# Kernel tuning notes

Hardware: AMD Instinct MI355X
Metric: run time of the kernel (lower is better)

The kernel has to match this reference:

```python
import jax, jax.numpy as jnp
import numpy as np

VOCAB, EMB, VGG, HID, LAYERS, B, T = 10000, 512, 4096, 512, 2, 128, 25


def setup_inputs() -> dict:
    key = jax.random.key(0)
    ks = jax.random.split(key, 20)
    n0 = HID + EMB   # layer-0 concat size
    n1 = HID + HID   # layer-1 concat size
    inp = {
        "vgg_fc7_features": jax.random.normal(ks[0], (B, VGG), jnp.float32),
        "xTokens": jax.random.randint(ks[1], (B, T), 0, VOCAB),
        "is_train": 1,
        "emb": jax.random.normal(ks[2], (VOCAB, EMB), jnp.float32) * 0.1,
        "W_in": jax.random.normal(ks[3], (VGG, HID), jnp.float32) / np.sqrt(VGG).astype(np.float32),
        "b_in": jnp.zeros((HID,), jnp.float32),
        "Wu0": jax.random.normal(ks[4], (n0, HID), jnp.float32) / np.sqrt(n0).astype(np.float32),
        "bu0": jnp.zeros((HID,), jnp.float32),
        "Wr0": jax.random.normal(ks[5], (n0, HID), jnp.float32) / np.sqrt(n0).astype(np.float32),
        "br0": jnp.zeros((HID,), jnp.float32),
        "Wc0": jax.random.normal(ks[6], (n0, HID), jnp.float32) / np.sqrt(n0).astype(np.float32),
        "bc0": jnp.zeros((HID,), jnp.float32),
        "Wu1": jax.random.normal(ks[7], (n1, HID), jnp.float32) / np.sqrt(n1).astype(np.float32),
        "bu1": jnp.zeros((HID,), jnp.float32),
        "Wr1": jax.random.normal(ks[8], (n1, HID), jnp.float32) / np.sqrt(n1).astype(np.float32),
        "br1": jnp.zeros((HID,), jnp.float32),
        "Wc1": jax.random.normal(ks[9], (n1, HID), jnp.float32) / np.sqrt(n1).astype(np.float32),
        "bc1": jnp.zeros((HID,), jnp.float32),
        "W_out": jax.random.normal(ks[10], (HID, VOCAB), jnp.float32) / np.sqrt(HID).astype(np.float32),
        "b_out": jnp.zeros((VOCAB,), jnp.float32),
    }
    return inp


def _gru(x, h, Wu, bu, Wr, br, Wc, bc):
    xh = jnp.concatenate([x, h], axis=1)
    gu = jax.nn.sigmoid(xh @ Wu + bu)
    gr = jax.nn.sigmoid(xh @ Wr + br)
    hh = jnp.tanh(jnp.concatenate([x, gr * h], axis=1) @ Wc + bc)
    return gu * h + (1.0 - gu) * hh


def reference(vgg_fc7_features, xTokens, is_train, emb, W_in, b_in,
              Wu0, bu0, Wr0, br0, Wc0, bc0,
              Wu1, bu1, Wr1, br1, Wc1, bc1,
              W_out, b_out):
    # initial hidden state from image features, replicated per rnn layer
    h0 = jnp.tanh(vgg_fc7_features @ W_in + b_in)  # [B, HID]
    init = (h0, h0)
    emb_seq = emb[xTokens]               # [B, T, EMB]
    emb_seq = jnp.swapaxes(emb_seq, 0, 1)  # [T, B, EMB]

    def step(carry, x_t):
        s0, s1 = carry
        s0n = _gru(x_t, s0, Wu0, bu0, Wr0, br0, Wc0, bc0)
        s1n = _gru(s0n, s1, Wu1, bu1, Wr1, br1, Wc1, bc1)
        logit = s1n @ W_out + b_out      # [B, VOCAB]
        return (s0n, s1n), logit

    (s0f, s1f), logits = jax.lax.scan(step, init, emb_seq)
    logits = jnp.swapaxes(logits, 0, 1)  # [B, T, VOCAB]
    current_state = jnp.stack([s0f, s1f])  # [LAYERS, B, HID]
    return logits, current_state
```

## Files before the change

### kernel.cpp

```cpp
#include <hip/hip_runtime.h>
#include <hip/hip_bf16.h>

#define BB 128
#define TT 25
#define VOCAB 10000
#define HIDD 512

typedef __hip_bfloat16 bf16;
typedef short bf16x8 __attribute__((ext_vector_type(8)));
typedef float f32x4 __attribute__((ext_vector_type(4)));

__device__ __forceinline__ float sigmoidf_(float x) { return 1.0f / (1.0f + __expf(-x)); }

__device__ __forceinline__ float4 f4_fma(float s, float4 w, float4 a) {
    a.x += s * w.x; a.y += s * w.y; a.z += s * w.z; a.w += s * w.w;
    return a;
}

__device__ __forceinline__ unsigned short f2bfu(float x) {
    bf16 h = __float2bfloat16(x);
    return *reinterpret_cast<unsigned short*>(&h);
}

__device__ __forceinline__ float4 core128(const float* __restrict__ Wp,
                                          const float* __restrict__ arow)
{
    float4 acc = {0.f, 0.f, 0.f, 0.f};
    #pragma unroll 2
    for (int k = 0; k < 128; k += 8) {
        float4 w[8];
        #pragma unroll
        for (int j = 0; j < 8; ++j)
            w[j] = *(const float4*)(Wp + (size_t)(k + j) * 512);
        #pragma unroll
        for (int j = 0; j < 8; ++j)
            acc = f4_fma(arow[k + j], w[j], acc);
    }
    return acc;
}

#define PHASE_REDUCE(SVAR) \
    __syncthreads(); \
    float4 SVAR; \
    if (tid < 32) { \
        SVAR = red[tid]; \
        _Pragma("unroll") \
        for (int j = 1; j < 8; ++j) { \
            float4 p = red[tid + 32 * j]; \
            SVAR.x += p.x; SVAR.y += p.y; SVAR.z += p.z; SVAR.w += p.w; \
        } \
    }

__global__ __launch_bounds__(256) void k_h0p(const float* __restrict__ A,
                                             const float* __restrict__ W,
                                             float* __restrict__ partial)
{
    __shared__ float As2[2][1032];
    __shared__ float4 red[256];
    const int tid = threadIdx.x;
    const int n4 = tid & 15, mi = (tid >> 4) & 1, kh = tid >> 5;
    const int m0 = blockIdx.y * 2, col0 = blockIdx.x * 64, kq = blockIdx.z;

    #pragma unroll
    for (int l = 0; l < 2; ++l) {
        int idx = tid + l * 256;
        int r = idx >> 8, c4 = (idx & 255) * 4;
        *(float4*)&As2[r][c4] =
            *(const float4*)&A[(size_t)(m0 + r) * 4096 + kq * 1024 + c4];
    }
    __syncthreads();
    red[tid] = core128(W + (size_t)(kq * 1024 + kh * 128) * 512 + col0 + n4 * 4,
                       &As2[mi][kh * 128]);
    PHASE_REDUCE(s)
    if (tid < 32) {
        int m = m0 + (tid >> 4), cc = col0 + (tid & 15) * 4;
        *(float4*)&partial[((size_t)kq * 128 + m) * 512 + cc] = s;
    }
}

__global__ void k_h0f(const float* __restrict__ partial,
                      const float* __restrict__ bias,
                      float* __restrict__ s0, float* __restrict__ s1)
{
    int i = blockIdx.x * 256 + threadIdx.x;
    size_t e = (size_t)i * 4;
    int cc = (int)(e & 511);
    float4 s = *(const float4*)&partial[e];
    #pragma unroll
    for (int j = 1; j < 4; ++j) {
        float4 p = *(const float4*)&partial[(size_t)j * 128 * 512 + e];
        s.x += p.x; s.y += p.y; s.z += p.z; s.w += p.w;
    }
    float4 b4 = *(const float4*)&bias[cc];
    float4 o;
    o.x = tanhf(s.x + b4.x); o.y = tanhf(s.y + b4.y);
    o.z = tanhf(s.z + b4.z); o.w = tanhf(s.w + b4.w);
    *(float4*)&s0[e] = o;
    *(float4*)&s1[e] = o;
}

__global__ __launch_bounds__(512, 4) void k_gates(
    const float* __restrict__ h0p, const float* __restrict__ h1p,
    const int* __restrict__ toks, const float* __restrict__ emb, int t,
    const float* __restrict__ Wu0, const float* __restrict__ bu0,
    const float* __restrict__ Wr0, const float* __restrict__ br0,
    const float* __restrict__ Wu1, const float* __restrict__ bu1,
    const float* __restrict__ Wr1, const float* __restrict__ br1,
    float* __restrict__ gu0, float* __restrict__ grh0,
    float* __restrict__ gu1, float* __restrict__ grh1,
    int doL0, int doL1)
{
    __shared__ float As[8 * 1028];
    __shared__ float4 red[8][8][16];
    const int bx = blockIdx.x;
    const int cb = bx & 7, gate = (bx >> 3) & 3, mb = bx >> 5;
    if (gate < 2) { if (!doL0) return; } else { if (!doL1) return; }
    const int col0 = cb * 64, m0 = mb * 8;
    const int tid = threadIdx.x;

    #pragma unroll
    for (int l = 0; l < 4; ++l) {
        int idx = tid + l * 512;
        int r2 = idx >> 7;
        int c4 = (idx & 127) * 4;
        int r = r2 & 7, half = r2 >> 3;
        float4 v;
        if (gate < 2) {
            if (half == 0) {
                int tok = toks[(m0 + r) * TT + t];
                v = *(const float4*)&emb[(size_t)tok * 512 + c4];
            } else {
                v = *(const float4*)&h0p[(size_t)(m0 + r) * 512 + c4];
            }
        } else {
            const float* src = (half == 0) ? h0p : h1p;
            v = *(const float4*)&src[(size_t)(m0 + r) * 512 + c4];
        }
        *(float4*)&As[r * 1028 + half * 512 + c4] = v;
    }
    __syncthreads();

    {
        const int kq = tid >> 6, lane = tid & 63;
        const int n4 = lane & 15, rl = lane >> 4;
        const int col = col0 + n4 * 4;
        const float* W = gate == 0 ? Wu0 : gate == 1 ? Wr0 : gate == 2 ? Wu1 : Wr1;
        const float* wp = W + col + (size_t)kq * 128 * 512;
        const float* ap0 = As + rl * 1028 + kq * 128;
        const float* ap1 = As + (rl + 4) * 1028 + kq * 128;
        float4 acc0a = {0.f,0.f,0.f,0.f}, acc0b = {0.f,0.f,0.f,0.f};
        float4 acc1a = {0.f,0.f,0.f,0.f}, acc1b = {0.f,0.f,0.f,0.f};
        #pragma unroll 2
        for (int j = 0; j < 32; ++j) {
            float4 a0 = *(const float4*)(ap0 + j * 4);
            float4 a1 = *(const float4*)(ap1 + j * 4);
            float4 w0 = *(const float4*)(wp + (j * 4 + 0) * 512);
            float4 w1 = *(const float4*)(wp + (j * 4 + 1) * 512);
            float4 w2 = *(const float4*)(wp + (j * 4 + 2) * 512);
            float4 w3 = *(const float4*)(wp + (j * 4 + 3) * 512);
            acc0a = f4_fma(a0.x, w0, acc0a); acc1a = f4_fma(a1.x, w0, acc1a);
            acc0b = f4_fma(a0.y, w1, acc0b); acc1b = f4_fma(a1.y, w1, acc1b);
            acc0a = f4_fma(a0.z, w2, acc0a); acc1a = f4_fma(a1.z, w2, acc1a);
            acc0b = f4_fma(a0.w, w3, acc0b); acc1b = f4_fma(a1.w, w3, acc1b);
        }
        float4 s0v, s1v;
        s0v.x = acc0a.x + acc0b.x; s0v.y = acc0a.y + acc0b.y;
        s0v.z = acc0a.z + acc0b.z; s0v.w = acc0a.w + acc0b.w;
        s1v.x = acc1a.x + acc1b.x; s1v.y = acc1a.y + acc1b.y;
        s1v.z = acc1a.z + acc1b.z; s1v.w = acc1a.w + acc1b.w;
        red[kq][rl][n4] = s0v;
        red[kq][rl + 4][n4] = s1v;
    }
    __syncthreads();

    if (tid < 128) {
        const int row = tid >> 4, n4 = tid & 15;
        float4 s = red[0][row][n4];
        #pragma unroll
        for (int kq = 1; kq < 8; ++kq) {
            float4 p = red[kq][row][n4];
            s.x += p.x; s.y += p.y; s.z += p.z; s.w += p.w;
        }
        const int col = col0 + n4 * 4;
        const int m = m0 + row;
        const float* bias = gate == 0 ? bu0 : gate == 1 ? br0 : gate == 2 ? bu1 : br1;
        float4 b4 = *(const float4*)&bias[col];
        float4 o;
        o.x = sigmoidf_(s.x + b4.x); o.y = sigmoidf_(s.y + b4.y);
        o.z = sigmoidf_(s.z + b4.z); o.w = sigmoidf_(s.w + b4.w);
        size_t ofs = (size_t)m * 512 + col;
        if (gate == 1) {
            float4 h = *(const float4*)&h0p[ofs];
            o.x *= h.x; o.y *= h.y; o.z *= h.z; o.w *= h.w;
        } else if (gate == 3) {
            float4 h = *(const float4*)&h1p[ofs];
            o.x *= h.x; o.y *= h.y; o.z *= h.z; o.w *= h.w;
        }
        float* outp = gate == 0 ? gu0 : gate == 1 ? grh0 : gate == 2 ? gu1 : grh1;
        *(float4*)&outp[ofs] = o;
    }
}

__global__ __launch_bounds__(512, 2) void k_cand(
    const float* __restrict__ h0p, const float* __restrict__ h1p,
    float* __restrict__ h0c, float* __restrict__ h1c,
    const int* __restrict__ toks, const float* __restrict__ emb,
    int t0, int t1,
    const float* __restrict__ Wc0, const float* __restrict__ bc0,
    const float* __restrict__ Wc1, const float* __restrict__ bc1,
    const float* __restrict__ gu0, const float* __restrict__ grh0,
    const float* __restrict__ gu1, const float* __restrict__ grh1,
    unsigned short* __restrict__ s1bf, float* __restrict__ outS,
    int doL0, int doL1)
{
    __shared__ float As[8 * 1028];
    __shared__ float4 red[8][8][16];
    const int bx = blockIdx.x;
    const int cb = bx & 7, gate = (bx >> 3) & 1, mb = bx >> 4;
    if (gate == 0) { if (!doL0) return; } else { if (!doL1) return; }
    const int col0 = cb * 64, m0 = mb * 8;
    const int tid = threadIdx.x;

    #pragma unroll
    for (int l = 0; l < 4; ++l) {
        int idx = tid + l * 512;
        int r2 = idx >> 7;
        int c4 = (idx & 127) * 4;
        int r = r2 & 7, half = r2 >> 3;
        float4 v;
        if (gate == 0) {
            if (half == 0) {
                int tok = toks[(m0 + r) * TT + t0];
                v = *(const float4*)&emb[(size_t)tok * 512 + c4];
            } else {
                v = *(const float4*)&grh0[(size_t)(m0 + r) * 512 + c4];
            }
        } else {
            const float* src = (half == 0) ? h0p : grh1;
            v = *(const float4*)&src[(size_t)(m0 + r) * 512 + c4];
        }
        *(float4*)&As[r * 1028 + half * 512 + c4] = v;
    }
    __syncthreads();

    {
        const int kq = tid >> 6, lane = tid & 63;
        const int n4 = lane & 15, rl = lane >> 4;
        const int col = col0 + n4 * 4;
        const float* W = gate ? Wc1 : Wc0;
        const float* wp = W + col + (size_t)kq * 128 * 512;
        const float* ap0 = As + rl * 1028 + kq * 128;
        const float* ap1 = As + (rl + 4) * 1028 + kq * 128;
        float4 acc0a = {0.f,0.f,0.f,0.f}, acc0b = {0.f,0.f,0.f,0.f};
        float4 acc1a = {0.f,0.f,0.f,0.f}, acc1b = {0.f,0.f,0.f,0.f};
        #pragma unroll 2
        for (int j = 0; j < 32; ++j) {
            float4 a0 = *(const float4*)(ap0 + j * 4);
            float4 a1 = *(const float4*)(ap1 + j * 4);
            float4 w0 = *(const float4*)(wp + (j * 4 + 0) * 512);
            float4 w1 = *(const float4*)(wp + (j * 4 + 1) * 512);
            float4 w2 = *(const float4*)(wp + (j * 4 + 2) * 512);
            float4 w3 = *(const float4*)(wp + (j * 4 + 3) * 512);
            acc0a = f4_fma(a0.x, w0, acc0a); acc1a = f4_fma(a1.x, w0, acc1a);
            acc0b = f4_fma(a0.y, w1, acc0b); acc1b = f4_fma(a1.y, w1, acc1b);
            acc0a = f4_fma(a0.z, w2, acc0a); acc1a = f4_fma(a1.z, w2, acc1a);
            acc0b = f4_fma(a0.w, w3, acc0b); acc1b = f4_fma(a1.w, w3, acc1b);
        }
        float4 s0v, s1v;
        s0v.x = acc0a.x + acc0b.x; s0v.y = acc0a.y + acc0b.y;
        s0v.z = acc0a.z + acc0b.z; s0v.w = acc0a.w + acc0b.w;
        s1v.x = acc1a.x + acc1b.x; s1v.y = acc1a.y + acc1b.y;
        s1v.z = acc1a.z + acc1b.z; s1v.w = acc1a.w + acc1b.w;
        red[kq][rl][n4] = s0v;
        red[kq][rl + 4][n4] = s1v;
    }
    __syncthreads();

    if (tid < 128) {
        const int row = tid >> 4, n4 = tid & 15;
        float4 s = red[0][row][n4];
        #pragma unroll
        for (int kq = 1; kq < 8; ++kq) {
            float4 p = red[kq][row][n4];
            s.x += p.x; s.y += p.y; s.z += p.z; s.w += p.w;
        }
        const int col = col0 + n4 * 4;
        const int m = m0 + row;
        const float* bias = gate ? bc1 : bc0;
        float4 b4 = *(const float4*)&bias[col];
        size_t ofs = (size_t)m * 512 + col;
        float4 g  = *(const float4*)&((gate ? gu1 : gu0)[ofs]);
        float4 hv = *(const float4*)&((gate ? h1p : h0p)[ofs]);
        float4 o;
        o.x = g.x * hv.x + (1.f - g.x) * tanhf(s.x + b4.x);
        o.y = g.y * hv.y + (1.f - g.y) * tanhf(s.y + b4.y);
        o.z = g.z * hv.z + (1.f - g.z) * tanhf(s.z + b4.z);
        o.w = g.w * hv.w + (1.f - g.w) * tanhf(s.w + b4.w);
        *(float4*)&((gate ? h1c : h0c)[ofs]) = o;
        if (gate == 1) {
            ushort4 u;
            u.x = f2bfu(o.x); u.y = f2bfu(o.y); u.z = f2bfu(o.z); u.w = f2bfu(o.w);
            *(ushort4*)&s1bf[(size_t)t1 * BB * HIDD + ofs] = u;
            if (t1 == TT - 1)
                *(float4*)&outS[(size_t)BB * HIDD + ofs] = o;
        } else if (t0 == TT - 1) {
            *(float4*)&outS[ofs] = o;
        }
    }
}

__global__ __launch_bounds__(256) void k_wT(const float* __restrict__ W,
                                            unsigned short* __restrict__ wT)
{
    __shared__ float T[32][33];
    const int tid = threadIdx.x;
    const int n0 = blockIdx.x * 32, k0 = blockIdx.y * 32;
    {
        int r = tid >> 3, c4 = (tid & 7) * 4;
        float4 v = {0.f, 0.f, 0.f, 0.f};
        if (n0 + c4 + 3 < VOCAB)
            v = *(const float4*)&W[(size_t)(k0 + r) * VOCAB + n0 + c4];
        else {
            if (n0 + c4 + 0 < VOCAB) v.x = W[(size_t)(k0 + r) * VOCAB + n0 + c4 + 0];
            if (n0 + c4 + 1 < VOCAB) v.y = W[(size_t)(k0 + r) * VOCAB + n0 + c4 + 1];
            if (n0 + c4 + 2 < VOCAB) v.z = W[(size_t)(k0 + r) * VOCAB + n0 + c4 + 2];
        }
        T[r][c4 + 0] = v.x; T[r][c4 + 1] = v.y; T[r][c4 + 2] = v.z; T[r][c4 + 3] = v.w;
    }
    __syncthreads();
    {
        int rn = tid >> 3, c4 = (tid & 7) * 4;
        if (n0 + rn < VOCAB) {
            ushort4 u;
            u.x = f2bfu(T[c4 + 0][rn]);
            u.y = f2bfu(T[c4 + 1][rn]);
            u.z = f2bfu(T[c4 + 2][rn]);
            u.w = f2bfu(T[c4 + 3][rn]);
            *(ushort4*)&wT[(size_t)(n0 + rn) * 512 + k0 + c4] = u;
        }
    }
}

__global__ __launch_bounds__(256) void k_logits(const unsigned short* __restrict__ A,
                                                const unsigned short* __restrict__ Bt,
                                                const float* __restrict__ bias,
                                                float* __restrict__ out)
{
    __shared__ unsigned short As16[128][40];
    __shared__ unsigned short Bs16[128][40];
    const int tid = threadIdx.x;
    const int lane = tid & 63, w = tid >> 6;
    const int quad = lane >> 4, l15 = lane & 15;
    const int bid = blockIdx.x;
    const int xcd = bid & 7;
    const int rest = bid >> 3;
    const int mb = rest % 25;
    const int nb = (rest / 25) * 8 + xcd;
    if (nb >= 79) return;
    const int n0 = nb * 128, m0 = mb * 128;

    f32x4 acc[8][2];
    #pragma unroll
    for (int i = 0; i < 8; ++i)
        #pragma unroll
        for (int j = 0; j < 2; ++j) acc[i][j] = (f32x4){0.f, 0.f, 0.f, 0.f};

    ushort4 pa[4], pb[4];
    #pragma unroll
    for (int l = 0; l < 4; ++l) {
        int idx = tid + l * 256;
        int r = idx >> 3, c8 = (idx & 7) * 4;
        pa[l] = *(const ushort4*)&A[(size_t)(m0 + r) * 512 + c8];
        ushort4 bv = {0, 0, 0, 0};
        if (n0 + r < VOCAB)
            bv = *(const ushort4*)&Bt[(size_t)(n0 + r) * 512 + c8];
        pb[l] = bv;
    }

    for (int k0 = 0; k0 < 512; k0 += 32) {
        #pragma unroll
        for (int l = 0; l < 4; ++l) {
            int idx = tid + l * 256;
            int r = idx >> 3, c8 = (idx & 7) * 4;
            *(ushort4*)&As16[r][c8] = pa[l];
            *(ushort4*)&Bs16[r][c8] = pb[l];
        }
        if (k0 + 32 < 512) {
            #pragma unroll
            for (int l = 0; l < 4; ++l) {
                int idx = tid + l * 256;
                int r = idx >> 3, c8 = (idx & 7) * 4;
                pa[l] = *(const ushort4*)&A[(size_t)(m0 + r) * 512 + k0 + 32 + c8];
                ushort4 bv = {0, 0, 0, 0};
                if (n0 + r < VOCAB)
                    bv = *(const ushort4*)&Bt[(size_t)(n0 + r) * 512 + k0 + 32 + c8];
                pb[l] = bv;
            }
        }
        __syncthreads();
        bf16x8 bfrag[2];
        #pragma unroll
        for (int nt = 0; nt < 2; ++nt)
            bfrag[nt] = *(const bf16x8*)&Bs16[w * 32 + nt * 16 + l15][quad * 8];
        #pragma unroll
        for (int mt = 0; mt < 8; ++mt) {
            bf16x8 afrag = *(const bf16x8*)&As16[mt * 16 + l15][quad * 8];
            acc[mt][0] = __builtin_amdgcn_mfma_f32_16x16x32_bf16(afrag, bfrag[0], acc[mt][0], 0, 0, 0);
            acc[mt][1] = __builtin_amdgcn_mfma_f32_16x16x32_bf16(afrag, bfrag[1], acc[mt][1], 0, 0, 0);
        }
        __syncthreads();
    }

    #pragma unroll
    for (int nt = 0; nt < 2; ++nt) {
        int n = n0 + w * 32 + nt * 16 + l15;
        if (n < VOCAB) {
            float bo = bias[n];
            #pragma unroll
            for (int mt = 0; mt < 8; ++mt) {
                #pragma unroll
                for (int r = 0; r < 4; ++r) {
                    int m = m0 + mt * 16 + quad * 4 + r;
                    int tt = m >> 7, bb = m & 127;
                    out[(size_t)bb * (TT * VOCAB) + (size_t)tt * VOCAB + n] =
                        acc[mt][nt][r] + bo;
                }
            }
        }
    }
}

extern "C" void kernel_launch(void* const* d_in, const int* in_sizes, int n_in,
                              void* d_out, int out_size, void* d_ws, size_t ws_size,
                              hipStream_t stream)
{
    const float* vgg  = (const float*)d_in[0];
    const int*   toks = (const int*)d_in[1];
    const float* emb  = (const float*)d_in[3];
    const float* Win  = (const float*)d_in[4];
    const float* bin  = (const float*)d_in[5];
    const float* Wu0  = (const float*)d_in[6];
    const float* bu0  = (const float*)d_in[7];
    const float* Wr0  = (const float*)d_in[8];
    const float* br0  = (const float*)d_in[9];
    const float* Wc0  = (const float*)d_in[10];
    const float* bc0  = (const float*)d_in[11];
    const float* Wu1  = (const float*)d_in[12];
    const float* bu1  = (const float*)d_in[13];
    const float* Wr1  = (const float*)d_in[14];
    const float* br1  = (const float*)d_in[15];
    const float* Wc1  = (const float*)d_in[16];
    const float* bc1  = (const float*)d_in[17];
    const float* Wout = (const float*)d_in[18];
    const float* bout = (const float*)d_in[19];

    const size_t S = (size_t)BB * HIDD;
    float* ws = (float*)d_ws;
    float* h0b[2] = {ws,         ws + S};
    float* h1b[2] = {ws + 2 * S, ws + 3 * S};
    float* gu0  = ws + 4 * S;
    float* grh0 = ws + 5 * S;
    float* gu1  = ws + 6 * S;
    float* grh1 = ws + 7 * S;
    unsigned short* s1bf = (unsigned short*)(ws + 8 * S);
    unsigned short* wT   = s1bf + (size_t)TT * BB * HIDD;

    float* out = (float*)d_out;
    float* outS = out + (size_t)TT * BB * VOCAB;

    k_wT<<<dim3(313, 16), 256, 0, stream>>>(Wout, wT);
    k_h0p<<<dim3(8, 64, 4), 256, 0, stream>>>(vgg, Win, gu0);
    k_h0f<<<dim3(64), 256, 0, stream>>>(gu0, bin, h0b[1], h1b[1]);

    for (int i = 0; i <= TT; ++i) {
        int doL0 = (i < TT), doL1 = (i >= 1);
        const float* h0p_ = h0b[(i + 1) & 1];
        float*       h0c_ = h0b[i & 1];
        const float* h1p_ = h1b[i & 1];
        float*       h1c_ = h1b[(i + 1) & 1];

        k_gates<<<dim3(512), 512, 0, stream>>>(h0p_, h1p_, toks, emb, i,
                                               Wu0, bu0, Wr0, br0,
                                               Wu1, bu1, Wr1, br1,
                                               gu0, grh0, gu1, grh1,
                                               doL0, doL1);
        k_cand<<<dim3(256), 512, 0, stream>>>(h0p_, h1p_, h0c_, h1c_,
                                              toks, emb, i, i - 1,
                                              Wc0, bc0, Wc1, bc1,
                                              gu0, grh0, gu1, grh1,
                                              s1bf, outS, doL0, doL1);
    }

    k_logits<<<dim3(2000), 256, 0, stream>>>(s1bf, wT, bout, out);
}
```

Before: 1.086 ms.

## Precompute layer-0 input projections for all timesteps with a bf16 MFMA GEMM

Hoists the embedding-side half of the layer-0 GRU matmuls (update, reset, candidate) out of the recurrent loop into a single batched bf16 MFMA GEMM over all timesteps, storing the results in a workspace buffer. The per-step gate and candidate kernels then only multiply the hidden-state half for layer 0 and add the precomputed term, and the FMA loops are re-tiled so each thread handles one row and 8 columns. It also switches the logits and precompute stores to nontemporal and raises k_cand occupancy bounds. This trades fp32 precision on the input projection for bf16 and adds extra workspace and setup kernels, in exchange for shorter serial per-step work.

```diff
diff --git a/kernel.cpp b/kernel.cpp
--- a/kernel.cpp
+++ b/kernel.cpp
@@ -99,9 +99,121 @@
     *(float4*)&s1[e] = o;
 }
 
+__global__ __launch_bounds__(256) void k_xbf(const int* __restrict__ toks,
+                                             const float* __restrict__ emb,
+                                             unsigned short* __restrict__ xbf)
+{
+    int i = (blockIdx.x * 256 + threadIdx.x) * 4;
+    int row = i >> 9, col = i & 511;
+    int b = row & 127, tt = row >> 7;
+    int tok = toks[b * TT + tt];
+    float4 v = *(const float4*)&emb[(size_t)tok * 512 + col];
+    ushort4 u;
+    u.x = f2bfu(v.x); u.y = f2bfu(v.y); u.z = f2bfu(v.z); u.w = f2bfu(v.w);
+    *(ushort4*)&xbf[(size_t)row * 512 + col] = u;
+}
+
+__global__ __launch_bounds__(256) void k_wxT3(const float* __restrict__ Wu,
+                                              const float* __restrict__ Wr,
+                                              const float* __restrict__ Wc,
+                                              unsigned short* __restrict__ wxT)
+{
+    __shared__ float T[32][33];
+    const int tid = threadIdx.x;
+    const int n0 = blockIdx.x * 32, k0 = blockIdx.y * 32, g = blockIdx.z;
+    const float* W = g == 0 ? Wu : g == 1 ? Wr : Wc;
+    {
+        int r = tid >> 3, c4 = (tid & 7) * 4;
+        float4 v = *(const float4*)&W[(size_t)(k0 + r) * 512 + n0 + c4];
+        T[r][c4 + 0] = v.x; T[r][c4 + 1] = v.y; T[r][c4 + 2] = v.z; T[r][c4 + 3] = v.w;
+    }
+    __syncthreads();
+    {
+        int rn = tid >> 3, c4 = (tid & 7) * 4;
+        ushort4 u;
+        u.x = f2bfu(T[c4 + 0][rn]);
+        u.y = f2bfu(T[c4 + 1][rn]);
+        u.z = f2bfu(T[c4 + 2][rn]);
+        u.w = f2bfu(T[c4 + 3][rn]);
+        *(ushort4*)&wxT[(size_t)(g * 512 + n0 + rn) * 512 + k0 + c4] = u;
+    }
+}
+
+__global__ __launch_bounds__(256) void k_pre(const unsigned short* __restrict__ A,
+                                             const unsigned short* __restrict__ Bt,
+                                             float* __restrict__ out)
+{
+    __shared__ unsigned short As16[128][40];
+    __shared__ unsigned short Bs16[128][40];
+    const int tid = threadIdx.x;
+    const int lane = tid & 63, w = tid >> 6;
+    const int quad = lane >> 4, l15 = lane & 15;
+    const int n0 = blockIdx.x * 128, m0 = blockIdx.y * 128;
+
+    f32x4 acc[8][2];
+    #pragma unroll
+    for (int i = 0; i < 8; ++i)
+        #pragma unroll
+        for (int j = 0; j < 2; ++j) acc[i][j] = (f32x4){0.f, 0.f, 0.f, 0.f};
+
+    ushort4 pa[4], pb[4];
+    #pragma unroll
+    for (int l = 0; l < 4; ++l) {
+        int idx = tid + l * 256;
+        int r = idx >> 3, c8 = (idx & 7) * 4;
+        pa[l] = *(const ushort4*)&A[(size_t)(m0 + r) * 512 + c8];
+        pb[l] = *(const ushort4*)&Bt[(size_t)(n0 + r) * 512 + c8];
+    }
+
+    for (int k0 = 0; k0 < 512; k0 += 32) {
+        #pragma unroll
+        for (int l = 0; l < 4; ++l) {
+            int idx = tid + l * 256;
+            int r = idx >> 3, c8 = (idx & 7) * 4;
+            *(ushort4*)&As16[r][c8] = pa[l];
+            *(ushort4*)&Bs16[r][c8] = pb[l];
+        }
+        if (k0 + 32 < 512) {
+            #pragma unroll
+            for (int l = 0; l < 4; ++l) {
+                int idx = tid + l * 256;
+                int r = idx >> 3, c8 = (idx & 7) * 4;
+                pa[l] = *(const ushort4*)&A[(size_t)(m0 + r) * 512 + k0 + 32 + c8];
+                pb[l] = *(const ushort4*)&Bt[(size_t)(n0 + r) * 512 + k0 + 32 + c8];
+            }
+        }
+        __syncthreads();
+        bf16x8 bfrag[2];
+        #pragma unroll
+        for (int nt = 0; nt < 2; ++nt)
+            bfrag[nt] = *(const bf16x8*)&Bs16[w * 32 + nt * 16 + l15][quad * 8];
+        #pragma unroll
+        for (int mt = 0; mt < 8; ++mt) {
+            bf16x8 afrag = *(const bf16x8*)&As16[mt * 16 + l15][quad * 8];
+            acc[mt][0] = __builtin_amdgcn_mfma_f32_16x16x32_bf16(afrag, bfrag[0], acc[mt][0], 0, 0, 0);
+            acc[mt][1] = __builtin_amdgcn_mfma_f32_16x16x32_bf16(afrag, bfrag[1], acc[mt][1], 0, 0, 0);
+        }
+        __syncthreads();
+    }
+
+    #pragma unroll
+    for (int nt = 0; nt < 2; ++nt) {
+        int n = n0 + w * 32 + nt * 16 + l15;
+        #pragma unroll
+        for (int mt = 0; mt < 8; ++mt) {
+            #pragma unroll
+            for (int r = 0; r < 4; ++r) {
+                int m = m0 + mt * 16 + quad * 4 + r;
+                __builtin_nontemporal_store(acc[mt][nt][r],
+                                            &out[(size_t)m * 1536 + n]);
+            }
+        }
+    }
+}
+
 __global__ __launch_bounds__(512, 4) void k_gates(
     const float* __restrict__ h0p, const float* __restrict__ h1p,
-    const int* __restrict__ toks, const float* __restrict__ emb, int t,
+    const float* __restrict__ pre, int t,
     const float* __restrict__ Wu0, const float* __restrict__ bu0,
     const float* __restrict__ Wr0, const float* __restrict__ br0,
     const float* __restrict__ Wu1, const float* __restrict__ bu1,
@@ -117,59 +229,64 @@
     if (gate < 2) { if (!doL0) return; } else { if (!doL1) return; }
     const int col0 = cb * 64, m0 = mb * 8;
     const int tid = threadIdx.x;
-
-    #pragma unroll
-    for (int l = 0; l < 4; ++l) {
-        int idx = tid + l * 512;
-        int r2 = idx >> 7;
-        int c4 = (idx & 127) * 4;
-        int r = r2 & 7, half = r2 >> 3;
-        float4 v;
-        if (gate < 2) {
-            if (half == 0) {
-                int tok = toks[(m0 + r) * TT + t];
-                v = *(const float4*)&emb[(size_t)tok * 512 + c4];
-            } else {
-                v = *(const float4*)&h0p[(size_t)(m0 + r) * 512 + c4];
-            }
-        } else {
-            const float* src = (half == 0) ? h0p : h1p;
-            v = *(const float4*)&src[(size_t)(m0 + r) * 512 + c4];
-        }
-        *(float4*)&As[r * 1028 + half * 512 + c4] = v;
+    const int L0 = gate < 2;
+
+    if (L0) {
+        #pragma unroll
+        for (int l = 0; l < 2; ++l) {
+            int idx = tid + l * 512;
+            int r = idx >> 7, c4 = (idx & 127) * 4;
+            *(float4*)&As[r * 1028 + c4] =
+                *(const float4*)&h0p[(size_t)(m0 + r) * 512 + c4];
+        }
+    } else {
+        #pragma unroll
+        for (int l = 0; l < 4; ++l) {
+            int idx = tid + l * 512;
+            int r2 = idx >> 7, c4 = (idx & 127) * 4;
+            int r = r2 & 7, half = r2 >> 3;
+            const float* src = half ? h1p : h0p;
+            *(float4*)&As[r * 1028 + half * 512 + c4] =
+                *(const float4*)&src[(size_t)(m0 + r) * 512 + c4];
+        }
     }
     __syncthreads();
 
     {
-        const int kq = tid >> 6, lane = tid & 63;
-        const int n4 = lane & 15, rl = lane >> 4;
-        const int col = col0 + n4 * 4;
+        const int wv = tid >> 6, lane = tid & 63;
+        const int r = lane >> 3, cg = lane & 7;
+        const int Kw = L0 ? 64 : 128;
+        const int nj = Kw >> 2;
         const float* W = gate == 0 ? Wu0 : gate == 1 ? Wr0 : gate == 2 ? Wu1 : Wr1;
-        const float* wp = W + col + (size_t)kq * 128 * 512;
-        const float* ap0 = As + rl * 1028 + kq * 128;
-        const float* ap1 = As + (rl + 4) * 1028 + kq * 128;
-        float4 acc0a = {0.f,0.f,0.f,0.f}, acc0b = {0.f,0.f,0.f,0.f};
-        float4 acc1a = {0.f,0.f,0.f,0.f}, acc1b = {0.f,0.f,0.f,0.f};
+        const int wrow0 = (L0 ? 512 : 0) + wv * Kw;
+        const float* wp = W + (size_t)wrow0 * 512 + col0 + cg * 8;
+        const float* ap = As + r * 1028 + wv * Kw;
+        float4 aAa = {0,0,0,0}, aAb = {0,0,0,0};
+        float4 aBa = {0,0,0,0}, aBb = {0,0,0,0};
         #pragma unroll 2
-        for (int j = 0; j < 32; ++j) {
-            float4 a0 = *(const float4*)(ap0 + j * 4);
-            float4 a1 = *(const float4*)(ap1 + j * 4);
-            float4 w0 = *(const float4*)(wp + (j * 4 + 0) * 512);
-            float4 w1 = *(const float4*)(wp + (j * 4 + 1) * 512);
-            float4 w2 = *(const float4*)(wp + (j * 4 + 2) * 512);
-            float4 w3 = *(const float4*)(wp + (j * 4 + 3) * 512);
-            acc0a = f4_fma(a0.x, w0, acc0a); acc1a = f4_fma(a1.x, w0, acc1a);
-            acc0b = f4_fma(a0.y, w1, acc0b); acc1b = f4_fma(a1.y, w1, acc1b);
-            acc0a = f4_fma(a0.z, w2, acc0a); acc1a = f4_fma(a1.z, w2, acc1a);
-            acc0b = f4_fma(a0.w, w3, acc0b); acc1b = f4_fma(a1.w, w3, acc1b);
-        }
-        float4 s0v, s1v;
-        s0v.x = acc0a.x + acc0b.x; s0v.y = acc0a.y + acc0b.y;
-        s0v.z = acc0a.z + acc0b.z; s0v.w = acc0a.w + acc0b.w;
-        s1v.x = acc1a.x + acc1b.x; s1v.y = acc1a.y + acc1b.y;
-        s1v.z = acc1a.z + acc1b.z; s1v.w = acc1a.w + acc1b.w;
-        red[kq][rl][n4] = s0v;
-        red[kq][rl + 4][n4] = s1v;
+        for (int j = 0; j < nj; ++j) {
+            float4 a4 = *(const float4*)(ap + j * 4);
+            const float* wj = wp + (size_t)j * 2048;
+            float4 w0a = *(const float4*)(wj);
+            float4 w0b = *(const float4*)(wj + 4);
+            float4 w1a = *(const float4*)(wj + 512);
+            float4 w1b = *(const float4*)(wj + 516);
+            float4 w2a = *(const float4*)(wj + 1024);
+            float4 w2b = *(const float4*)(wj + 1028);
+            float4 w3a = *(const float4*)(wj + 1536);
+            float4 w3b = *(const float4*)(wj + 1540);
+            aAa = f4_fma(a4.x, w0a, aAa); aAb = f4_fma(a4.x, w0b, aAb);
+            aBa = f4_fma(a4.y, w1a, aBa); aBb = f4_fma(a4.y, w1b, aBb);
+            aAa = f4_fma(a4.z, w2a, aAa); aAb = f4_fma(a4.z, w2b, aAb);
+            aBa = f4_fma(a4.w, w3a, aBa); aBb = f4_fma(a4.w, w3b, aBb);
+        }
+        float4 sa, sb;
+        sa.x = aAa.x + aBa.x; sa.y = aAa.y + aBa.y;
+        sa.z = aAa.z + aBa.z; sa.w = aAa.w + aBa.w;
+        sb.x = aAb.x + aBb.x; sb.y = aAb.y + aBb.y;
+        sb.z = aAb.z + aBb.z; sb.w = aAb.w + aBb.w;
+        red[wv][r][cg * 2]     = sa;
+        red[wv][r][cg * 2 + 1] = sb;
     }
     __syncthreads();
 
@@ -183,6 +300,11 @@
         }
         const int col = col0 + n4 * 4;
         const int m = m0 + row;
+        if (L0) {
+            float4 p4 = *(const float4*)&pre[((size_t)t * 128 + m) * 1536
+                                             + gate * 512 + col];
+            s.x += p4.x; s.y += p4.y; s.z += p4.z; s.w += p4.w;
+        }
         const float* bias = gate == 0 ? bu0 : gate == 1 ? br0 : gate == 2 ? bu1 : br1;
         float4 b4 = *(const float4*)&bias[col];
         float4 o;
@@ -201,11 +323,10 @@
     }
 }
 
-__global__ __launch_bounds__(512, 2) void k_cand(
+__global__ __launch_bounds__(512, 4) void k_cand(
     const float* __restrict__ h0p, const float* __restrict__ h1p,
     float* __restrict__ h0c, float* __restrict__ h1c,
-    const int* __restrict__ toks, const float* __restrict__ emb,
-    int t0, int t1,
+    const float* __restrict__ pre, int t0, int t1,
     const float* __restrict__ Wc0, const float* __restrict__ bc0,
     const float* __restrict__ Wc1, const float* __restrict__ bc1,
     const float* __restrict__ gu0, const float* __restrict__ grh0,
@@ -220,59 +341,64 @@
     if (gate == 0) { if (!doL0) return; } else { if (!doL1) return; }
     const int col0 = cb * 64, m0 = mb * 8;
     const int tid = threadIdx.x;
-
-    #pragma unroll
-    for (int l = 0; l < 4; ++l) {
-        int idx = tid + l * 512;
-        int r2 = idx >> 7;
-        int c4 = (idx & 127) * 4;
-        int r = r2 & 7, half = r2 >> 3;
-        float4 v;
-        if (gate == 0) {
-            if (half == 0) {
-                int tok = toks[(m0 + r) * TT + t0];
-                v = *(const float4*)&emb[(size_t)tok * 512 + c4];
-            } else {
-                v = *(const float4*)&grh0[(size_t)(m0 + r) * 512 + c4];
-            }
-        } else {
-            const float* src = (half == 0) ? h0p : grh1;
-            v = *(const float4*)&src[(size_t)(m0 + r) * 512 + c4];
-        }
-        *(float4*)&As[r * 1028 + half * 512 + c4] = v;
+    const int L0 = gate == 0;
+
+    if (L0) {
+        #pragma unroll
+        for (int l = 0; l < 2; ++l) {
+            int idx = tid + l * 512;
+            int r = idx >> 7, c4 = (idx & 127) * 4;
+            *(float4*)&As[r * 1028 + c4] =
+                *(const float4*)&grh0[(size_t)(m0 + r) * 512 + c4];
+        }
+    } else {
+        #pragma unroll
+        for (int l = 0; l < 4; ++l) {
+            int idx = tid + l * 512;
+            int r2 = idx >> 7, c4 = (idx & 127) * 4;
+            int r = r2 & 7, half = r2 >> 3;
+            const float* src = half ? grh1 : h0p;
+            *(float4*)&As[r * 1028 + half * 512 + c4] =
+                *(const float4*)&src[(size_t)(m0 + r) * 512 + c4];
+        }
     }
     __syncthreads();
 
     {
-        const int kq = tid >> 6, lane = tid & 63;
-        const int n4 = lane & 15, rl = lane >> 4;
-        const int col = col0 + n4 * 4;
-        const float* W = gate ? Wc1 : Wc0;
-        const float* wp = W + col + (size_t)kq * 128 * 512;
-        const float* ap0 = As + rl * 1028 + kq * 128;
-        const float* ap1 = As + (rl + 4) * 1028 + kq * 128;
-        float4 acc0a = {0.f,0.f,0.f,0.f}, acc0b = {0.f,0.f,0.f,0.f};
-        float4 acc1a = {0.f,0.f,0.f,0.f}, acc1b = {0.f,0.f,0.f,0.f};
+        const int wv = tid >> 6, lane = tid & 63;
+        const int r = lane >> 3, cg = lane & 7;
+        const int Kw = L0 ? 64 : 128;
+        const int nj = Kw >> 2;
+        const float* W = L0 ? Wc0 : Wc1;
+        const int wrow0 = (L0 ? 512 : 0) + wv * Kw;
+        const float* wp = W + (size_t)wrow0 * 512 + col0 + cg * 8;
+        const float* ap = As + r * 1028 + wv * Kw;
+        float4 aAa = {0,0,0,0}, aAb = {0,0,0,0};
+        float4 aBa = {0,0,0,0}, aBb = {0,0,0,0};
         #pragma unroll 2
-        for (int j = 0; j < 32; ++j) {
-            float4 a0 = *(const float4*)(ap0 + j * 4);
-            float4 a1 = *(const float4*)(ap1 + j * 4);
-            float4 w0 = *(const float4*)(wp + (j * 4 + 0) * 512);
-            float4 w1 = *(const float4*)(wp + (j * 4 + 1) * 512);
-            float4 w2 = *(const float4*)(wp + (j * 4 + 2) * 512);
-            float4 w3 = *(const float4*)(wp + (j * 4 + 3) * 512);
-            acc0a = f4_fma(a0.x, w0, acc0a); acc1a = f4_fma(a1.x, w0, acc1a);
-            acc0b = f4_fma(a0.y, w1, acc0b); acc1b = f4_fma(a1.y, w1, acc1b);
-            acc0a = f4_fma(a0.z, w2, acc0a); acc1a = f4_fma(a1.z, w2, acc1a);
-            acc0b = f4_fma(a0.w, w3, acc0b); acc1b = f4_fma(a1.w, w3, acc1b);
-        }
-        float4 s0v, s1v;
-        s0v.x = acc0a.x + acc0b.x; s0v.y = acc0a.y + acc0b.y;
-        s0v.z = acc0a.z + acc0b.z; s0v.w = acc0a.w + acc0b.w;
-        s1v.x = acc1a.x + acc1b.x; s1v.y = acc1a.y + acc1b.y;
-        s1v.z = acc1a.z + acc1b.z; s1v.w = acc1a.w + acc1b.w;
-        red[kq][rl][n4] = s0v;
-        red[kq][rl + 4][n4] = s1v;
+        for (int j = 0; j < nj; ++j) {
+            float4 a4 = *(const float4*)(ap + j * 4);
+            const float* wj = wp + (size_t)j * 2048;
+            float4 w0a = *(const float4*)(wj);
+            float4 w0b = *(const float4*)(wj + 4);
+            float4 w1a = *(const float4*)(wj + 512);
+            float4 w1b = *(const float4*)(wj + 516);
+            float4 w2a = *(const float4*)(wj + 1024);
+            float4 w2b = *(const float4*)(wj + 1028);
+            float4 w3a = *(const float4*)(wj + 1536);
+            float4 w3b = *(const float4*)(wj + 1540);
+            aAa = f4_fma(a4.x, w0a, aAa); aAb = f4_fma(a4.x, w0b, aAb);
+            aBa = f4_fma(a4.y, w1a, aBa); aBb = f4_fma(a4.y, w1b, aBb);
+            aAa = f4_fma(a4.z, w2a, aAa); aAb = f4_fma(a4.z, w2b, aAb);
+            aBa = f4_fma(a4.w, w3a, aBa); aBb = f4_fma(a4.w, w3b, aBb);
+        }
+        float4 sa, sb;
+        sa.x = aAa.x + aBa.x; sa.y = aAa.y + aBa.y;
+        sa.z = aAa.z + aBa.z; sa.w = aAa.w + aBa.w;
+        sb.x = aAb.x + aBb.x; sb.y = aAb.y + aBb.y;
+        sb.z = aAb.z + aBb.z; sb.w = aAb.w + aBb.w;
+        red[wv][r][cg * 2]     = sa;
+        red[wv][r][cg * 2 + 1] = sb;
     }
     __syncthreads();
 
@@ -286,18 +412,23 @@
         }
         const int col = col0 + n4 * 4;
         const int m = m0 + row;
-        const float* bias = gate ? bc1 : bc0;
+        if (L0) {
+            float4 p4 = *(const float4*)&pre[((size_t)t0 * 128 + m) * 1536
+                                             + 1024 + col];
+            s.x += p4.x; s.y += p4.y; s.z += p4.z; s.w += p4.w;
+        }
+        const float* bias = L0 ? bc0 : bc1;
         float4 b4 = *(const float4*)&bias[col];
         size_t ofs = (size_t)m * 512 + col;
-        float4 g  = *(const float4*)&((gate ? gu1 : gu0)[ofs]);
-        float4 hv = *(const float4*)&((gate ? h1p : h0p)[ofs]);
+        float4 g  = *(const float4*)&((L0 ? gu0 : gu1)[ofs]);
+        float4 hv = *(const float4*)&((L0 ? h0p : h1p)[ofs]);
         float4 o;
         o.x = g.x * hv.x + (1.f - g.x) * tanhf(s.x + b4.x);
         o.y = g.y * hv.y + (1.f - g.y) * tanhf(s.y + b4.y);
         o.z = g.z * hv.z + (1.f - g.z) * tanhf(s.z + b4.z);
         o.w = g.w * hv.w + (1.f - g.w) * tanhf(s.w + b4.w);
-        *(float4*)&((gate ? h1c : h0c)[ofs]) = o;
-        if (gate == 1) {
+        *(float4*)&((L0 ? h0c : h1c)[ofs]) = o;
+        if (!L0) {
             ushort4 u;
             u.x = f2bfu(o.x); u.y = f2bfu(o.y); u.z = f2bfu(o.z); u.w = f2bfu(o.w);
             *(ushort4*)&s1bf[(size_t)t1 * BB * HIDD + ofs] = u;
@@ -422,8 +553,8 @@
                 for (int r = 0; r < 4; ++r) {
                     int m = m0 + mt * 16 + quad * 4 + r;
                     int tt = m >> 7, bb = m & 127;
-                    out[(size_t)bb * (TT * VOCAB) + (size_t)tt * VOCAB + n] =
-                        acc[mt][nt][r] + bo;
+                    __builtin_nontemporal_store(acc[mt][nt][r] + bo,
+                        &out[(size_t)bb * (TT * VOCAB) + (size_t)tt * VOCAB + n]);
                 }
             }
         }
@@ -464,6 +595,9 @@
     float* grh1 = ws + 7 * S;
     unsigned short* s1bf = (unsigned short*)(ws + 8 * S);
     unsigned short* wT   = s1bf + (size_t)TT * BB * HIDD;
+    unsigned short* xbf  = wT + (size_t)VOCAB * HIDD;
+    unsigned short* wxT  = xbf + (size_t)TT * BB * HIDD;
+    float* pre = (float*)(wxT + (size_t)1536 * HIDD);
 
     float* out = (float*)d_out;
     float* outS = out + (size_t)TT * BB * VOCAB;
@@ -471,6 +605,9 @@
     k_wT<<<dim3(313, 16), 256, 0, stream>>>(Wout, wT);
     k_h0p<<<dim3(8, 64, 4), 256, 0, stream>>>(vgg, Win, gu0);
     k_h0f<<<dim3(64), 256, 0, stream>>>(gu0, bin, h0b[1], h1b[1]);
+    k_xbf<<<dim3(1600), 256, 0, stream>>>(toks, emb, xbf);
+    k_wxT3<<<dim3(16, 16, 3), 256, 0, stream>>>(Wu0, Wr0, Wc0, wxT);
+    k_pre<<<dim3(12, 25), 256, 0, stream>>>(xbf, wxT, pre);
 
     for (int i = 0; i <= TT; ++i) {
         int doL0 = (i < TT), doL1 = (i >= 1);
@@ -479,13 +616,13 @@
         const float* h1p_ = h1b[i & 1];
         float*       h1c_ = h1b[(i + 1) & 1];
 
-        k_gates<<<dim3(512), 512, 0, stream>>>(h0p_, h1p_, toks, emb, i,
+        k_gates<<<dim3(512), 512, 0, stream>>>(h0p_, h1p_, pre, i,
                                                Wu0, bu0, Wr0, br0,
                                                Wu1, bu1, Wr1, br1,
                                                gu0, grh0, gu1, grh1,
                                                doL0, doL1);
         k_cand<<<dim3(256), 512, 0, stream>>>(h0p_, h1p_, h0c_, h1c_,
-                                              toks, emb, i, i - 1,
+                                              pre, i, i - 1,
                                               Wc0, bc0, Wc1, bc1,
                                               gu0, grh0, gu1, grh1,
                                               s1bf, outS, doL0, doL1);
```

New measurement: 1.603 ms. 1.48x slower.
